# Kernel tuning notes

Measured on AMD Instinct MI355X. Metric: run time of the kernel, lower is better.

## Reference

```python
import jax, jax.numpy as jnp
import numpy as np

SCALE = 100.0
ALPHA_MEM = 0.9
ALPHA_P = 0.99
ALPHA_MEM_OUT = 0.9

@jax.custom_vjp
def spike(x):
    return (x > 0).astype(x.dtype)

def _spike_fwd(x):
    return spike(x), x

def _spike_bwd(x, g):
    return (g / (SCALE * jnp.abs(x) + 1.0) ** 2,)

spike.defvjp(_spike_fwd, _spike_bwd)

B, T, N_IN, N, N_OUT = 64, 200, 128, 2048, 20

def setup_inputs() -> dict:
    key = jax.random.key(0)
    ks = jax.random.split(key, 6)
    inputs = jax.random.normal(ks[0], (B, T, N_IN), dtype=jnp.float32)
    w = jax.random.normal(ks[1], (N, N), dtype=jnp.float32) / np.sqrt(N)
    wscale_in = 1.0 - ALPHA_MEM
    w_in = jax.random.normal(ks[2], (N_IN, N), dtype=jnp.float32) * (wscale_in / np.sqrt(N_IN))
    wscale_out = 1.0 - ALPHA_MEM_OUT
    w_out = jax.random.normal(ks[3], (N, N_OUT), dtype=jnp.float32) * (wscale_out / np.sqrt(N))
    w_signs = jnp.sign(jax.random.normal(ks[4], (N,), dtype=jnp.float32))
    p = 0.1 * jax.random.normal(ks[5], (N,), dtype=jnp.float32)
    return {"inputs": inputs, "w": w, "w_in": w_in, "w_out": w_out,
            "w_signs": w_signs, "p": p}

def reference(inputs, w, w_in, w_out, w_signs, p):
    dt = inputs.dtype
    h1 = jnp.einsum('btc,cn->btn', inputs, w_in)          # [B,T,N]
    rec_w = w_signs[:, None] * jnp.abs(w)                  # [N,N]
    depr = (p < 0).astype(dt)                              # [N]

    def step(carry, h1_t):
        mem, w_p = carry
        mthr = mem - 1.0
        out = spike(mthr)
        rst = jax.lax.stop_gradient((mthr > 0).astype(dt))
        syn_p = jnp.einsum('bn,no->bo', out * (1.0 + w_p), rec_w)
        w_p_new = w_p * ALPHA_P + out * p * (1.0 + depr * w_p)
        mem_new = ALPHA_MEM * mem + h1_t + syn_p - rst
        return (mem_new, w_p_new), out

    zeros = jnp.zeros((h1.shape[0], rec_w.shape[0]), dtype=dt)
    _, spk = jax.lax.scan(step, (zeros, zeros), jnp.swapaxes(h1, 0, 1))
    spk_rec = jnp.swapaxes(spk, 0, 1)                      # [B,T,N]

    h2 = jnp.einsum('btn,no->bto', spk_rec, w_out)         # [B,T,O]

    def out_step(o, h2_t):
        o2 = ALPHA_MEM_OUT * o + h2_t
        return o2, o2

    o0 = jnp.zeros((h2.shape[0], h2.shape[2]), dtype=dt)
    _, outs = jax.lax.scan(out_step, o0, jnp.swapaxes(h2, 0, 1))
    return jnp.swapaxes(outs, 0, 1)                        # [B,T,O]
```

## Files before the change

### kernel.cpp

```cpp
#include <hip/hip_runtime.h>

#define BB   64
#define TT   200
#define NIN  128
#define NN   2048
#define NOUT 20

#define S    8
#define NWIN 25
#define ACAP 64
#define BCAP 128

typedef __attribute__((ext_vector_type(8))) short short8;
typedef __attribute__((ext_vector_type(4))) float f32x4;

__device__ __forceinline__ void bf16split(float x, ushort& h, ushort& l) {
    unsigned u = __float_as_uint(x);
    unsigned hb = (u + 0x7FFFu + ((u >> 16) & 1u)) >> 16;
    h = (ushort)hb;
    float xh = __uint_as_float(hb << 16);
    float xl = x - xh;
    unsigned v = __float_as_uint(xl);
    l = (ushort)((v + 0x7FFFu + ((v >> 16) & 1u)) >> 16);
}

__global__ __launch_bounds__(256) void repack_a(
    const float* __restrict__ X, ushort* __restrict__ Ap)
{
    const int blk  = blockIdx.x;
    const int tid  = threadIdx.x;
    const int kc   = tid >> 6;
    const int lane = tid & 63;
    const int lr   = lane & 15, lg = lane >> 4;

    const float* src = X + (size_t)(blk * 16 + lr) * NIN + kc * 32 + lg * 8;
    float f[8];
    *(float4*)(f)     = *(const float4*)(src);
    *(float4*)(f + 4) = *(const float4*)(src + 4);

    short8 hv, lv;
    #pragma unroll
    for (int j = 0; j < 8; ++j) {
        ushort h, l;
        bf16split(f[j], h, l);
        hv[j] = (short)h; lv[j] = (short)l;
    }
    ushort* dst = Ap + (size_t)(blk * 4 + kc) * 1024 + lane * 8;
    *(short8*)(dst)       = hv;
    *(short8*)(dst + 512) = lv;
}

__global__ __launch_bounds__(256) void repack_b(
    const float* __restrict__ W, ushort* __restrict__ Bp)
{
    const int blk  = blockIdx.x;
    const int tid  = threadIdx.x;
    const int kc   = tid >> 6;
    const int lane = tid & 63;
    const int lr   = lane & 15, lg = lane >> 4;

    const float* src = W + (size_t)(kc * 32 + lg * 8) * NN + blk * 16 + lr;
    float f[8];
    #pragma unroll
    for (int j = 0; j < 8; ++j) f[j] = src[(size_t)j * NN];

    short8 hv, lv;
    #pragma unroll
    for (int j = 0; j < 8; ++j) {
        ushort h, l;
        bf16split(f[j], h, l);
        hv[j] = (short)h; lv[j] = (short)l;
    }
    ushort* dst = Bp + (size_t)(blk * 4 + kc) * 1024 + lane * 8;
    *(short8*)(dst)       = hv;
    *(short8*)(dst + 512) = lv;
}

__global__ __launch_bounds__(256, 2) void h1_mfma(
    const ushort* __restrict__ Ap, const ushort* __restrict__ Bp,
    float* __restrict__ C)
{
    const int tid  = threadIdx.x;
    const int w_   = tid >> 6, lane = tid & 63;
    const int lr   = lane & 15, lg = lane >> 4;
    const int m0   = blockIdx.y * 128, n0 = blockIdx.x * 128;
    const int wr   = (w_ >> 1) * 64, wc = (w_ & 1) * 64;

    const ushort* pA = Ap + (size_t)((m0 + wr) >> 4) * 4096 + lane * 8;
    const ushort* pB = Bp + (size_t)((n0 + wc) >> 4) * 4096 + lane * 8;

#define LDF(p) (*(const short8*)(p))
    short8 ah[2][4], al[2][4], bh[2][4], bl[2][4];
    #pragma unroll
    for (int rb = 0; rb < 4; ++rb) {
        ah[0][rb] = LDF(pA + rb * 4096);
        al[0][rb] = LDF(pA + rb * 4096 + 512);
        bh[0][rb] = LDF(pB + rb * 4096);
        bl[0][rb] = LDF(pB + rb * 4096 + 512);
    }

    f32x4 acc[4][4];
    const f32x4 z = {0.f, 0.f, 0.f, 0.f};
    #pragma unroll
    for (int rb = 0; rb < 4; ++rb)
        #pragma unroll
        for (int cb = 0; cb < 4; ++cb) acc[rb][cb] = z;

    #pragma unroll
    for (int kc = 0; kc < 4; ++kc) {
        const int cur = kc & 1, nxt = cur ^ 1;
        if (kc < 3) {
            const int ko = (kc + 1) * 1024;
            #pragma unroll
            for (int rb = 0; rb < 4; ++rb) {
                ah[nxt][rb] = LDF(pA + rb * 4096 + ko);
                al[nxt][rb] = LDF(pA + rb * 4096 + ko + 512);
                bh[nxt][rb] = LDF(pB + rb * 4096 + ko);
                bl[nxt][rb] = LDF(pB + rb * 4096 + ko + 512);
            }
        }
        #pragma unroll
        for (int rb = 0; rb < 4; ++rb)
            #pragma unroll
            for (int cb = 0; cb < 4; ++cb) {
                acc[rb][cb] = __builtin_amdgcn_mfma_f32_16x16x32_bf16(
                    bh[cur][cb], ah[cur][rb], acc[rb][cb], 0, 0, 0);
                acc[rb][cb] = __builtin_amdgcn_mfma_f32_16x16x32_bf16(
                    bl[cur][cb], ah[cur][rb], acc[rb][cb], 0, 0, 0);
                acc[rb][cb] = __builtin_amdgcn_mfma_f32_16x16x32_bf16(
                    bh[cur][cb], al[cur][rb], acc[rb][cb], 0, 0, 0);
            }
    }
#undef LDF

    #pragma unroll
    for (int rb = 0; rb < 4; ++rb) {
        float* Crow = C + (size_t)(m0 + wr + rb * 16 + lr) * NN + n0 + wc + lg * 4;
        #pragma unroll
        for (int cb = 0; cb < 4; ++cb)
            *(f32x4*)(Crow + cb * 16) = acc[rb][cb];
    }
}

__global__ __launch_bounds__(512) void snn_scan(
    const float* __restrict__ h1, const float* __restrict__ w,
    const float* __restrict__ w_signs, const float* __restrict__ pvec,
    const float* __restrict__ w_out, float* __restrict__ out)
{
    const int b   = blockIdx.x;
    const int tid = threadIdx.x;
    const int n0  = tid << 2;

    __shared__ int   s_amask[2];
    __shared__ int   s_acnt[2][S];
    __shared__ int   s_aidx[2][S][ACAP];
    __shared__ float s_aval[2][S][ACAP];
    __shared__ int   s_bcnt[2];
    __shared__ int   s_bidx[2][BCAP];
    __shared__ float s_bval[2][BCAP];

    if (tid < 2) { s_amask[tid] = 0; s_bcnt[tid] = 0; }
    if (tid < 2 * S) ((int*)s_acnt)[tid] = 0;

    float4 mem = {0.f,0.f,0.f,0.f}, wp = {0.f,0.f,0.f,0.f};
    const float4 p4 = *(const float4*)(pvec + n0);
    const float4 sg = *(const float4*)(w_signs + n0);
    float4 depr;
    depr.x = (p4.x < 0.f) ? 1.f : 0.f;  depr.y = (p4.y < 0.f) ? 1.f : 0.f;
    depr.z = (p4.z < 0.f) ? 1.f : 0.f;  depr.w = (p4.w < 0.f) ? 1.f : 0.f;

    const float P99[S] = {1.0f, 0.99f, 0.9801f, 0.970299f, 0.96059601f,
                          0.9509900499f, 0.941480149401f, 0.93206534790699f};
    const float P99_8 = 0.9227446944279201f;

    const float* hb = h1 + (size_t)b * TT * NN + n0;
    float* outb = out + (size_t)b * TT * NOUT + tid;
    float o2 = 0.f;

    float4 PA[S], PB[S];
    #pragma unroll
    for (int j = 0; j < S; ++j) PA[j] = *(const float4*)(hb + (size_t)j * NN);
    __syncthreads();

#define RAWBAR()                                              \
    do { asm volatile("s_waitcnt lgkmcnt(0)" ::: "memory");   \
         __builtin_amdgcn_s_barrier();                        \
         asm volatile("" ::: "memory"); } while (0)

    auto window = [&](float4 (&Pc)[S], float4 (&Pf)[S], int wnd) {
        const int p  = wnd & 1;
        const int t0 = wnd * S;
        const float4 memB = mem, wpB = wp;

        #pragma unroll
        for (int j = 0; j < S; ++j) {
            const float4 a = Pc[j];
            int tp = t0 + j + S; if (tp > TT - 1) tp = TT - 1;
            Pf[j] = *(const float4*)(hb + (size_t)tp * NN);

            const float mx = fmaxf(fmaxf(mem.x, mem.y), fmaxf(mem.z, mem.w));
            if (__builtin_expect(mx > 1.f, 0)) {
                const bool f0 = mem.x > 1.f, f1 = mem.y > 1.f,
                           f2 = mem.z > 1.f, f3 = mem.w > 1.f;
                atomicOr(&s_amask[p], 1 << j);
                if (f0) { int k = atomicAdd(&s_acnt[p][j], 1);
                          if (k < ACAP) { s_aidx[p][j][k] = n0;
                                          s_aval[p][j][k] = (1.f + wp.x * P99[j]) * sg.x; } }
                if (f1) { int k = atomicAdd(&s_acnt[p][j], 1);
                          if (k < ACAP) { s_aidx[p][j][k] = n0 + 1;
                                          s_aval[p][j][k] = (1.f + wp.y * P99[j]) * sg.y; } }
                if (f2) { int k = atomicAdd(&s_acnt[p][j], 1);
                          if (k < ACAP) { s_aidx[p][j][k] = n0 + 2;
                                          s_aval[p][j][k] = (1.f + wp.z * P99[j]) * sg.z; } }
                if (f3) { int k = atomicAdd(&s_acnt[p][j], 1);
                          if (k < ACAP) { s_aidx[p][j][k] = n0 + 3;
                                          s_aval[p][j][k] = (1.f + wp.w * P99[j]) * sg.w; } }
                mem.x = fmaf(0.9f, mem.x, a.x) - (f0 ? 1.f : 0.f);
                mem.y = fmaf(0.9f, mem.y, a.y) - (f1 ? 1.f : 0.f);
                mem.z = fmaf(0.9f, mem.z, a.z) - (f2 ? 1.f : 0.f);
                mem.w = fmaf(0.9f, mem.w, a.w) - (f3 ? 1.f : 0.f);
            } else {
                mem.x = fmaf(0.9f, mem.x, a.x);
                mem.y = fmaf(0.9f, mem.y, a.y);
                mem.z = fmaf(0.9f, mem.z, a.z);
                mem.w = fmaf(0.9f, mem.w, a.w);
            }
        }

        RAWBAR();
        const int mask = s_amask[p];

        if (__builtin_expect(mask == 0, 1)) {
            wp.x *= P99_8; wp.y *= P99_8; wp.z *= P99_8; wp.w *= P99_8;
            if (tid < NOUT) {
                #pragma unroll
                for (int j = 0; j < S; ++j) {
                    o2 = 0.9f * o2;
                    outb[(size_t)(t0 + j) * NOUT] = o2;
                }
            }
            return;
        }

        const int tstar = __ffs(mask) - 1;
        mem = memB; wp = wpB;
        #pragma unroll
        for (int j = 0; j < S; ++j) {
            const float4 a = Pc[j];
            if (j < tstar) {
                mem.x = fmaf(0.9f, mem.x, a.x);
                mem.y = fmaf(0.9f, mem.y, a.y);
                mem.z = fmaf(0.9f, mem.z, a.z);
                mem.w = fmaf(0.9f, mem.w, a.w);
                wp.x *= 0.99f; wp.y *= 0.99f; wp.z *= 0.99f; wp.w *= 0.99f;
                if (tid < NOUT) { o2 = 0.9f * o2;
                                  outb[(size_t)(t0 + j) * NOUT] = o2; }
            } else if (j == tstar) {
                const bool f0 = mem.x > 1.f, f1 = mem.y > 1.f,
                           f2 = mem.z > 1.f, f3 = mem.w > 1.f;
                int cnt = s_acnt[p][j]; if (cnt > ACAP) cnt = ACAP;
                float4 syn = {0.f,0.f,0.f,0.f};
                for (int m = 0; m < cnt; ++m) {
                    const int nm = s_aidx[p][j][m];
                    const float vm = s_aval[p][j][m];
                    const float4 wr = *(const float4*)(w + (size_t)nm * NN + n0);
                    syn.x = fmaf(vm, fabsf(wr.x), syn.x);
                    syn.y = fmaf(vm, fabsf(wr.y), syn.y);
                    syn.z = fmaf(vm, fabsf(wr.z), syn.z);
                    syn.w = fmaf(vm, fabsf(wr.w), syn.w);
                }
                if (tid < NOUT) {
                    float c = 0.f;
                    for (int m = 0; m < cnt; ++m)
                        c += w_out[(size_t)s_aidx[p][j][m] * NOUT + tid];
                    o2 = 0.9f * o2 + c;
                    outb[(size_t)(t0 + j) * NOUT] = o2;
                }
                mem.x = fmaf(0.9f, mem.x, a.x) + syn.x - (f0 ? 1.f : 0.f);
                mem.y = fmaf(0.9f, mem.y, a.y) + syn.y - (f1 ? 1.f : 0.f);
                mem.z = fmaf(0.9f, mem.z, a.z) + syn.z - (f2 ? 1.f : 0.f);
                mem.w = fmaf(0.9f, mem.w, a.w) + syn.w - (f3 ? 1.f : 0.f);
                wp.x = f0 ? 0.99f*wp.x + p4.x*(1.f + depr.x*wp.x) : 0.99f*wp.x;
                wp.y = f1 ? 0.99f*wp.y + p4.y*(1.f + depr.y*wp.y) : 0.99f*wp.y;
                wp.z = f2 ? 0.99f*wp.z + p4.z*(1.f + depr.z*wp.z) : 0.99f*wp.z;
                wp.w = f3 ? 0.99f*wp.w + p4.w*(1.f + depr.w*wp.w) : 0.99f*wp.w;
            } else {
                const int par = j & 1;
                const bool f0 = mem.x > 1.f, f1 = mem.y > 1.f,
                           f2 = mem.z > 1.f, f3 = mem.w > 1.f;
                if (f0 | f1 | f2 | f3) {
                    if (f0) { int k = atomicAdd(&s_bcnt[par], 1); if (k < BCAP) {
                              s_bidx[par][k] = n0;     s_bval[par][k] = (1.f + wp.x) * sg.x; } }
                    if (f1) { int k = atomicAdd(&s_bcnt[par], 1); if (k < BCAP) {
                              s_bidx[par][k] = n0 + 1; s_bval[par][k] = (1.f + wp.y) * sg.y; } }
                    if (f2) { int k = atomicAdd(&s_bcnt[par], 1); if (k < BCAP) {
                              s_bidx[par][k] = n0 + 2; s_bval[par][k] = (1.f + wp.z) * sg.z; } }
                    if (f3) { int k = atomicAdd(&s_bcnt[par], 1); if (k < BCAP) {
                              s_bidx[par][k] = n0 + 3; s_bval[par][k] = (1.f + wp.w) * sg.w; } }
                }
                RAWBAR();
                int cnt = s_bcnt[par]; if (cnt > BCAP) cnt = BCAP;
                float4 syn = {0.f,0.f,0.f,0.f};
                for (int m = 0; m < cnt; ++m) {
                    const int nm = s_bidx[par][m];
                    const float vm = s_bval[par][m];
                    const float4 wr = *(const float4*)(w + (size_t)nm * NN + n0);
                    syn.x = fmaf(vm, fabsf(wr.x), syn.x);
                    syn.y = fmaf(vm, fabsf(wr.y), syn.y);
                    syn.z = fmaf(vm, fabsf(wr.z), syn.z);
                    syn.w = fmaf(vm, fabsf(wr.w), syn.w);
                }
                if (tid < NOUT) {
                    float c = 0.f;
                    for (int m = 0; m < cnt; ++m)
                        c += w_out[(size_t)s_bidx[par][m] * NOUT + tid];
                    o2 = 0.9f * o2 + c;
                    outb[(size_t)(t0 + j) * NOUT] = o2;
                }
                mem.x = fmaf(0.9f, mem.x, a.x) + syn.x - (f0 ? 1.f : 0.f);
                mem.y = fmaf(0.9f, mem.y, a.y) + syn.y - (f1 ? 1.f : 0.f);
                mem.z = fmaf(0.9f, mem.z, a.z) + syn.z - (f2 ? 1.f : 0.f);
                mem.w = fmaf(0.9f, mem.w, a.w) + syn.w - (f3 ? 1.f : 0.f);
                wp.x = f0 ? 0.99f*wp.x + p4.x*(1.f + depr.x*wp.x) : 0.99f*wp.x;
                wp.y = f1 ? 0.99f*wp.y + p4.y*(1.f + depr.y*wp.y) : 0.99f*wp.y;
                wp.z = f2 ? 0.99f*wp.z + p4.z*(1.f + depr.z*wp.z) : 0.99f*wp.z;
                wp.w = f3 ? 0.99f*wp.w + p4.w*(1.f + depr.w*wp.w) : 0.99f*wp.w;
                RAWBAR();
                if (tid == 0) s_bcnt[par] = 0;
            }
        }
        RAWBAR();
        if (tid < S) s_acnt[p][tid] = 0;
        else if (tid == S) s_amask[p] = 0;
    };

    for (int wnd = 0; wnd < NWIN - 1; wnd += 2) {
        window(PA, PB, wnd);
        window(PB, PA, wnd + 1);
    }
    window(PA, PB, NWIN - 1);
#undef RAWBAR
}

extern "C" void kernel_launch(void* const* d_in, const int* in_sizes, int n_in,
                              void* d_out, int out_size, void* d_ws, size_t ws_size,
                              hipStream_t stream) {
    (void)in_sizes; (void)n_in; (void)out_size; (void)ws_size;
    const float* inputs  = (const float*)d_in[0];
    const float* w       = (const float*)d_in[1];
    const float* w_in    = (const float*)d_in[2];
    const float* w_out   = (const float*)d_in[3];
    const float* w_signs = (const float*)d_in[4];
    const float* p       = (const float*)d_in[5];
    float* out = (float*)d_out;

    const size_t H1B = (size_t)BB * TT * NN * 4;
    const size_t APB = (size_t)800 * 4096 * 2;

    float*  h1 = (float*)d_ws;
    ushort* Ap = (ushort*)((char*)d_ws + H1B);
    ushort* Bp = (ushort*)((char*)d_ws + H1B + APB);

    repack_a<<<800, 256, 0, stream>>>(inputs, Ap);
    repack_b<<<128, 256, 0, stream>>>(w_in, Bp);

    dim3 gg(NN / 128, (BB * TT) / 128);
    h1_mfma<<<gg, 256, 0, stream>>>(Ap, Bp, h1);

    snn_scan<<<BB, 512, 0, stream>>>(h1, w, w_signs, p, w_out, out);
}
```

Baseline: 99.60 us.

## Split each batch's SNN scan across four workgroups with global-memory sync

The recurrent scan for each batch is split across 4 workgroups of 128 threads, each owning 512 neurons, instead of one 512-thread workgroup per batch. Spike lists and counters move from shared memory to global buffers, and the workgroups synchronise per window and per spiking step through atomic counters with spin-waits. The aim is to use more compute units and shorten per-block work on the latency-bound scan. In exchange it adds inter-block spin barriers, global atomics and fences, and relies on all 256 blocks being co-resident.

```diff
diff --git a/kernel.cpp b/kernel.cpp
--- a/kernel.cpp
+++ b/kernel.cpp
@@ -8,11 +8,25 @@
 
 #define S    8
 #define NWIN 25
-#define ACAP 64
-#define BCAP 128
+#define NCHUNK 4
+#define NLOC 512
+#define STHREADS 128
+#define SACAP 32
+#define SBCAP 64
 
 typedef __attribute__((ext_vector_type(8))) short short8;
 typedef __attribute__((ext_vector_type(4))) float f32x4;
+
+#define W0 0
+#define AC 1600
+#define W2 52800
+#define BC 65600
+#define ZTOT (1600 + 51200 + 12800 + 51200)
+__device__ int   g_sync[ZTOT];
+__device__ int   g_aidx[64 * 2 * 8 * NCHUNK * SACAP];
+__device__ float g_aval[64 * 2 * 8 * NCHUNK * SACAP];
+__device__ int   g_bidx[64 * 2 * 8 * NCHUNK * SBCAP];
+__device__ float g_bval[64 * 2 * 8 * NCHUNK * SBCAP];
 
 __device__ __forceinline__ void bf16split(float x, ushort& h, ushort& l) {
     unsigned u = __float_as_uint(x);
@@ -27,6 +41,10 @@
 __global__ __launch_bounds__(256) void repack_a(
     const float* __restrict__ X, ushort* __restrict__ Ap)
 {
+    {
+        int i = blockIdx.x * 256 + threadIdx.x;
+        if (i < ZTOT) g_sync[i] = 0;
+    }
     const int blk  = blockIdx.x;
     const int tid  = threadIdx.x;
     const int kc   = tid >> 6;
@@ -142,25 +160,20 @@
     }
 }
 
-__global__ __launch_bounds__(512) void snn_scan(
+__global__ __launch_bounds__(STHREADS) void snn_scan(
     const float* __restrict__ h1, const float* __restrict__ w,
     const float* __restrict__ w_signs, const float* __restrict__ pvec,
     const float* __restrict__ w_out, float* __restrict__ out)
 {
-    const int b   = blockIdx.x;
+    const int bid = blockIdx.x;
+    const int ch  = bid >> 6;
+    const int b   = bid & 63;
     const int tid = threadIdx.x;
-    const int n0  = tid << 2;
-
-    __shared__ int   s_amask[2];
-    __shared__ int   s_acnt[2][S];
-    __shared__ int   s_aidx[2][S][ACAP];
-    __shared__ float s_aval[2][S][ACAP];
-    __shared__ int   s_bcnt[2];
-    __shared__ int   s_bidx[2][BCAP];
-    __shared__ float s_bval[2][BCAP];
-
-    if (tid < 2) { s_amask[tid] = 0; s_bcnt[tid] = 0; }
-    if (tid < 2 * S) ((int*)s_acnt)[tid] = 0;
+    const int n0  = ch * NLOC + (tid << 2);
+
+    __shared__ int s_amask;
+    __shared__ int s_gm3;
+    if (tid == 0) s_amask = 0;
 
     float4 mem = {0.f,0.f,0.f,0.f}, wp = {0.f,0.f,0.f,0.f};
     const float4 p4 = *(const float4*)(pvec + n0);
@@ -175,6 +188,7 @@
 
     const float* hb = h1 + (size_t)b * TT * NN + n0;
     float* outb = out + (size_t)b * TT * NOUT + tid;
+    const bool douto = (ch == 0) && (tid < NOUT);
     float o2 = 0.f;
 
     float4 PA[S], PB[S];
@@ -188,9 +202,11 @@
          asm volatile("" ::: "memory"); } while (0)
 
     auto window = [&](float4 (&Pc)[S], float4 (&Pf)[S], int wnd) {
-        const int p  = wnd & 1;
-        const int t0 = wnd * S;
+        const int p    = wnd & 1;
+        const int t0   = wnd * S;
+        const int widx = b * 25 + wnd;
         const float4 memB = mem, wpB = wp;
+        bool pushed = false;
 
         #pragma unroll
         for (int j = 0; j < S; ++j) {
@@ -202,19 +218,18 @@
             if (__builtin_expect(mx > 1.f, 0)) {
                 const bool f0 = mem.x > 1.f, f1 = mem.y > 1.f,
                            f2 = mem.z > 1.f, f3 = mem.w > 1.f;
-                atomicOr(&s_amask[p], 1 << j);
-                if (f0) { int k = atomicAdd(&s_acnt[p][j], 1);
-                          if (k < ACAP) { s_aidx[p][j][k] = n0;
-                                          s_aval[p][j][k] = (1.f + wp.x * P99[j]) * sg.x; } }
-                if (f1) { int k = atomicAdd(&s_acnt[p][j], 1);
-                          if (k < ACAP) { s_aidx[p][j][k] = n0 + 1;
-                                          s_aval[p][j][k] = (1.f + wp.y * P99[j]) * sg.y; } }
-                if (f2) { int k = atomicAdd(&s_acnt[p][j], 1);
-                          if (k < ACAP) { s_aidx[p][j][k] = n0 + 2;
-                                          s_aval[p][j][k] = (1.f + wp.z * P99[j]) * sg.z; } }
-                if (f3) { int k = atomicAdd(&s_acnt[p][j], 1);
-                          if (k < ACAP) { s_aidx[p][j][k] = n0 + 3;
-                                          s_aval[p][j][k] = (1.f + wp.w * P99[j]) * sg.w; } }
+                atomicOr(&s_amask, 1 << j);
+                int* cp = &g_sync[AC + (widx * 8 + j) * 4 + ch];
+                const int ab = ((((b * 2 + p) * 8 + j) * 4 + ch)) * SACAP;
+                if (f0) { int k = atomicAdd(cp, 1); if (k < SACAP) {
+                          g_aidx[ab+k] = n0;     g_aval[ab+k] = (1.f + wp.x * P99[j]) * sg.x; } }
+                if (f1) { int k = atomicAdd(cp, 1); if (k < SACAP) {
+                          g_aidx[ab+k] = n0 + 1; g_aval[ab+k] = (1.f + wp.y * P99[j]) * sg.y; } }
+                if (f2) { int k = atomicAdd(cp, 1); if (k < SACAP) {
+                          g_aidx[ab+k] = n0 + 2; g_aval[ab+k] = (1.f + wp.z * P99[j]) * sg.z; } }
+                if (f3) { int k = atomicAdd(cp, 1); if (k < SACAP) {
+                          g_aidx[ab+k] = n0 + 3; g_aval[ab+k] = (1.f + wp.w * P99[j]) * sg.w; } }
+                pushed = true;
                 mem.x = fmaf(0.9f, mem.x, a.x) - (f0 ? 1.f : 0.f);
                 mem.y = fmaf(0.9f, mem.y, a.y) - (f1 ? 1.f : 0.f);
                 mem.z = fmaf(0.9f, mem.z, a.z) - (f2 ? 1.f : 0.f);
@@ -227,12 +242,32 @@
             }
         }
 
+        if (pushed) __threadfence();
         RAWBAR();
-        const int mask = s_amask[p];
-
-        if (__builtin_expect(mask == 0, 1)) {
+
+        if (tid == 0) {
+            const int lm = s_amask;
+            s_amask = 0;
+            int lm3 = 0;
+            #pragma unroll
+            for (int j = 0; j < S; ++j) lm3 |= ((lm >> j) & 1) << (3 * j);
+            atomicAdd(&g_sync[W0 + widx], 1 + (lm3 << 8));
+            unsigned v; int it = 0;
+            for (;;) {
+                v = (unsigned)__hip_atomic_load(&g_sync[W0 + widx],
+                        __ATOMIC_ACQUIRE, __HIP_MEMORY_SCOPE_AGENT);
+                if ((v & 255u) == NCHUNK) break;
+                __builtin_amdgcn_s_sleep(2);
+                if (++it > (1 << 20)) break;
+            }
+            s_gm3 = (int)(v >> 8);
+        }
+        RAWBAR();
+        const int gm3 = s_gm3;
+
+        if (__builtin_expect(gm3 == 0, 1)) {
             wp.x *= P99_8; wp.y *= P99_8; wp.z *= P99_8; wp.w *= P99_8;
-            if (tid < NOUT) {
+            if (douto) {
                 #pragma unroll
                 for (int j = 0; j < S; ++j) {
                     o2 = 0.9f * o2;
@@ -242,7 +277,8 @@
             return;
         }
 
-        const int tstar = __ffs(mask) - 1;
+        __threadfence();
+        const int tstar = (__ffs(gm3) - 1) / 3;
         mem = memB; wp = wpB;
         #pragma unroll
         for (int j = 0; j < S; ++j) {
@@ -253,26 +289,29 @@
                 mem.z = fmaf(0.9f, mem.z, a.z);
                 mem.w = fmaf(0.9f, mem.w, a.w);
                 wp.x *= 0.99f; wp.y *= 0.99f; wp.z *= 0.99f; wp.w *= 0.99f;
-                if (tid < NOUT) { o2 = 0.9f * o2;
-                                  outb[(size_t)(t0 + j) * NOUT] = o2; }
+                if (douto) { o2 = 0.9f * o2;
+                             outb[(size_t)(t0 + j) * NOUT] = o2; }
             } else if (j == tstar) {
                 const bool f0 = mem.x > 1.f, f1 = mem.y > 1.f,
                            f2 = mem.z > 1.f, f3 = mem.w > 1.f;
-                int cnt = s_acnt[p][j]; if (cnt > ACAP) cnt = ACAP;
                 float4 syn = {0.f,0.f,0.f,0.f};
-                for (int m = 0; m < cnt; ++m) {
-                    const int nm = s_aidx[p][j][m];
-                    const float vm = s_aval[p][j][m];
-                    const float4 wr = *(const float4*)(w + (size_t)nm * NN + n0);
-                    syn.x = fmaf(vm, fabsf(wr.x), syn.x);
-                    syn.y = fmaf(vm, fabsf(wr.y), syn.y);
-                    syn.z = fmaf(vm, fabsf(wr.z), syn.z);
-                    syn.w = fmaf(vm, fabsf(wr.w), syn.w);
-                }
-                if (tid < NOUT) {
-                    float c = 0.f;
-                    for (int m = 0; m < cnt; ++m)
-                        c += w_out[(size_t)s_aidx[p][j][m] * NOUT + tid];
+                float c = 0.f;
+                for (int cc = 0; cc < NCHUNK; ++cc) {
+                    int cnt = g_sync[AC + (widx * 8 + j) * 4 + cc];
+                    if (cnt > SACAP) cnt = SACAP;
+                    const int rb2 = ((((b * 2 + p) * 8 + j) * 4 + cc)) * SACAP;
+                    for (int m = 0; m < cnt; ++m) {
+                        const int nm = g_aidx[rb2 + m];
+                        const float vm = g_aval[rb2 + m];
+                        const float4 wr = *(const float4*)(w + (size_t)nm * NN + n0);
+                        syn.x = fmaf(vm, fabsf(wr.x), syn.x);
+                        syn.y = fmaf(vm, fabsf(wr.y), syn.y);
+                        syn.z = fmaf(vm, fabsf(wr.z), syn.z);
+                        syn.w = fmaf(vm, fabsf(wr.w), syn.w);
+                        if (douto) c += w_out[(size_t)nm * NOUT + tid];
+                    }
+                }
+                if (douto) {
                     o2 = 0.9f * o2 + c;
                     outb[(size_t)(t0 + j) * NOUT] = o2;
                 }
@@ -285,35 +324,54 @@
                 wp.z = f2 ? 0.99f*wp.z + p4.z*(1.f + depr.z*wp.z) : 0.99f*wp.z;
                 wp.w = f3 ? 0.99f*wp.w + p4.w*(1.f + depr.w*wp.w) : 0.99f*wp.w;
             } else {
-                const int par = j & 1;
                 const bool f0 = mem.x > 1.f, f1 = mem.y > 1.f,
                            f2 = mem.z > 1.f, f3 = mem.w > 1.f;
-                if (f0 | f1 | f2 | f3) {
-                    if (f0) { int k = atomicAdd(&s_bcnt[par], 1); if (k < BCAP) {
-                              s_bidx[par][k] = n0;     s_bval[par][k] = (1.f + wp.x) * sg.x; } }
-                    if (f1) { int k = atomicAdd(&s_bcnt[par], 1); if (k < BCAP) {
-                              s_bidx[par][k] = n0 + 1; s_bval[par][k] = (1.f + wp.y) * sg.y; } }
-                    if (f2) { int k = atomicAdd(&s_bcnt[par], 1); if (k < BCAP) {
-                              s_bidx[par][k] = n0 + 2; s_bval[par][k] = (1.f + wp.z) * sg.z; } }
-                    if (f3) { int k = atomicAdd(&s_bcnt[par], 1); if (k < BCAP) {
-                              s_bidx[par][k] = n0 + 3; s_bval[par][k] = (1.f + wp.w) * sg.w; } }
+                const bool sp = f0 | f1 | f2 | f3;
+                if (sp) {
+                    int* cp = &g_sync[BC + (widx * 8 + j) * 4 + ch];
+                    const int bb = ((((b * 2 + p) * 8 + j) * 4 + ch)) * SBCAP;
+                    if (f0) { int k = atomicAdd(cp, 1); if (k < SBCAP) {
+                              g_bidx[bb+k] = n0;     g_bval[bb+k] = (1.f + wp.x) * sg.x; } }
+                    if (f1) { int k = atomicAdd(cp, 1); if (k < SBCAP) {
+                              g_bidx[bb+k] = n0 + 1; g_bval[bb+k] = (1.f + wp.y) * sg.y; } }
+                    if (f2) { int k = atomicAdd(cp, 1); if (k < SBCAP) {
+                              g_bidx[bb+k] = n0 + 2; g_bval[bb+k] = (1.f + wp.z) * sg.z; } }
+                    if (f3) { int k = atomicAdd(cp, 1); if (k < SBCAP) {
+                              g_bidx[bb+k] = n0 + 3; g_bval[bb+k] = (1.f + wp.w) * sg.w; } }
+                    __threadfence();
                 }
                 RAWBAR();
-                int cnt = s_bcnt[par]; if (cnt > BCAP) cnt = BCAP;
+                if (tid == 0) {
+                    atomicAdd(&g_sync[W2 + widx * 8 + j], 1);
+                    int it = 0;
+                    for (;;) {
+                        int v = __hip_atomic_load(&g_sync[W2 + widx * 8 + j],
+                                    __ATOMIC_ACQUIRE, __HIP_MEMORY_SCOPE_AGENT);
+                        if (v == NCHUNK) break;
+                        __builtin_amdgcn_s_sleep(2);
+                        if (++it > (1 << 20)) break;
+                    }
+                }
+                RAWBAR();
+                __threadfence();
                 float4 syn = {0.f,0.f,0.f,0.f};
-                for (int m = 0; m < cnt; ++m) {
-                    const int nm = s_bidx[par][m];
-                    const float vm = s_bval[par][m];
-                    const float4 wr = *(const float4*)(w + (size_t)nm * NN + n0);
-                    syn.x = fmaf(vm, fabsf(wr.x), syn.x);
-                    syn.y = fmaf(vm, fabsf(wr.y), syn.y);
-                    syn.z = fmaf(vm, fabsf(wr.z), syn.z);
-                    syn.w = fmaf(vm, fabsf(wr.w), syn.w);
-                }
-                if (tid < NOUT) {
-                    float c = 0.f;
-                    for (int m = 0; m < cnt; ++m)
-                        c += w_out[(size_t)s_bidx[par][m] * NOUT + tid];
+                float c = 0.f;
+                for (int cc = 0; cc < NCHUNK; ++cc) {
+                    int cnt = g_sync[BC + (widx * 8 + j) * 4 + cc];
+                    if (cnt > SBCAP) cnt = SBCAP;
+                    const int rb2 = ((((b * 2 + p) * 8 + j) * 4 + cc)) * SBCAP;
+                    for (int m = 0; m < cnt; ++m) {
+                        const int nm = g_bidx[rb2 + m];
+                        const float vm = g_bval[rb2 + m];
+                        const float4 wr = *(const float4*)(w + (size_t)nm * NN + n0);
+                        syn.x = fmaf(vm, fabsf(wr.x), syn.x);
+                        syn.y = fmaf(vm, fabsf(wr.y), syn.y);
+                        syn.z = fmaf(vm, fabsf(wr.z), syn.z);
+                        syn.w = fmaf(vm, fabsf(wr.w), syn.w);
+                        if (douto) c += w_out[(size_t)nm * NOUT + tid];
+                    }
+                }
+                if (douto) {
                     o2 = 0.9f * o2 + c;
                     outb[(size_t)(t0 + j) * NOUT] = o2;
                 }
@@ -325,13 +383,8 @@
                 wp.y = f1 ? 0.99f*wp.y + p4.y*(1.f + depr.y*wp.y) : 0.99f*wp.y;
                 wp.z = f2 ? 0.99f*wp.z + p4.z*(1.f + depr.z*wp.z) : 0.99f*wp.z;
                 wp.w = f3 ? 0.99f*wp.w + p4.w*(1.f + depr.w*wp.w) : 0.99f*wp.w;
-                RAWBAR();
-                if (tid == 0) s_bcnt[par] = 0;
             }
         }
-        RAWBAR();
-        if (tid < S) s_acnt[p][tid] = 0;
-        else if (tid == S) s_amask[p] = 0;
     };
 
     for (int wnd = 0; wnd < NWIN - 1; wnd += 2) {
@@ -367,5 +420,5 @@
     dim3 gg(NN / 128, (BB * TT) / 128);
     h1_mfma<<<gg, 256, 0, stream>>>(Ap, Bp, h1);
 
-    snn_scan<<<BB, 512, 0, stream>>>(h1, w, w_signs, p, w_out, out);
-}
+    snn_scan<<<BB * NCHUNK, STHREADS, 0, stream>>>(h1, w, w_signs, p, w_out, out);
+}
```

Measured after the change: 362.3 us. 3.64x slower.

## Fuse input GEMM and scan into one kernel with per-timestep-slab flag polling

Applied to the files above, without the earlier changes.

Merges the h1 GEMM and the recurrent scan into a single launch. The first 64 blocks run the per-batch scan and the remaining 800 compute GEMM tiles. h1 rows are reordered time-major so each 256-row GEMM slab covers 4 timesteps for all batches. GEMM blocks bump a global per-slab counter when done, and scan blocks spin-poll those counters before reading each window, so the scan can start while later timesteps are still being computed. This removes one launch and the serialisation between the two phases. It relies on the scan blocks being scheduled early, uses relaxed atomics with threadfence ordering, and has a bounded spin timeout that could read stale data if producers are delayed.

```diff
diff --git a/kernel.cpp b/kernel.cpp
--- a/kernel.cpp
+++ b/kernel.cpp
@@ -11,8 +11,12 @@
 #define ACAP 64
 #define BCAP 128
 
+#define HSTRIDE (64 * NN)
+
 typedef __attribute__((ext_vector_type(8))) short short8;
 typedef __attribute__((ext_vector_type(4))) float f32x4;
+
+__device__ int g_pcnt[64];
 
 __device__ __forceinline__ void bf16split(float x, ushort& h, ushort& l) {
     unsigned u = __float_as_uint(x);
@@ -27,13 +31,16 @@
 __global__ __launch_bounds__(256) void repack_a(
     const float* __restrict__ X, ushort* __restrict__ Ap)
 {
+    if (blockIdx.x == 0 && threadIdx.x < 64) g_pcnt[threadIdx.x] = 0;
     const int blk  = blockIdx.x;
     const int tid  = threadIdx.x;
     const int kc   = tid >> 6;
     const int lane = tid & 63;
     const int lr   = lane & 15, lg = lane >> 4;
 
-    const float* src = X + (size_t)(blk * 16 + lr) * NIN + kc * 32 + lg * 8;
+    const int r  = blk * 16 + lr;
+    const int bb = r & 63, tt = r >> 6;
+    const float* src = X + ((size_t)bb * TT + tt) * NIN + kc * 32 + lg * 8;
     float f[8];
     *(float4*)(f)     = *(const float4*)(src);
     *(float4*)(f + 4) = *(const float4*)(src + 4);
@@ -76,80 +83,91 @@
     *(short8*)(dst + 512) = lv;
 }
 
-__global__ __launch_bounds__(256, 2) void h1_mfma(
+__global__ __launch_bounds__(512, 2) void fused_gemm_scan(
     const ushort* __restrict__ Ap, const ushort* __restrict__ Bp,
-    float* __restrict__ C)
-{
-    const int tid  = threadIdx.x;
-    const int w_   = tid >> 6, lane = tid & 63;
-    const int lr   = lane & 15, lg = lane >> 4;
-    const int m0   = blockIdx.y * 128, n0 = blockIdx.x * 128;
-    const int wr   = (w_ >> 1) * 64, wc = (w_ & 1) * 64;
-
-    const ushort* pA = Ap + (size_t)((m0 + wr) >> 4) * 4096 + lane * 8;
-    const ushort* pB = Bp + (size_t)((n0 + wc) >> 4) * 4096 + lane * 8;
-
-#define LDF(p) (*(const short8*)(p))
-    short8 ah[2][4], al[2][4], bh[2][4], bl[2][4];
-    #pragma unroll
-    for (int rb = 0; rb < 4; ++rb) {
-        ah[0][rb] = LDF(pA + rb * 4096);
-        al[0][rb] = LDF(pA + rb * 4096 + 512);
-        bh[0][rb] = LDF(pB + rb * 4096);
-        bl[0][rb] = LDF(pB + rb * 4096 + 512);
-    }
-
-    f32x4 acc[4][4];
-    const f32x4 z = {0.f, 0.f, 0.f, 0.f};
-    #pragma unroll
-    for (int rb = 0; rb < 4; ++rb)
-        #pragma unroll
-        for (int cb = 0; cb < 4; ++cb) acc[rb][cb] = z;
-
-    #pragma unroll
-    for (int kc = 0; kc < 4; ++kc) {
-        const int cur = kc & 1, nxt = cur ^ 1;
-        if (kc < 3) {
-            const int ko = (kc + 1) * 1024;
-            #pragma unroll
-            for (int rb = 0; rb < 4; ++rb) {
-                ah[nxt][rb] = LDF(pA + rb * 4096 + ko);
-                al[nxt][rb] = LDF(pA + rb * 4096 + ko + 512);
-                bh[nxt][rb] = LDF(pB + rb * 4096 + ko);
-                bl[nxt][rb] = LDF(pB + rb * 4096 + ko + 512);
-            }
-        }
-        #pragma unroll
-        for (int rb = 0; rb < 4; ++rb)
-            #pragma unroll
-            for (int cb = 0; cb < 4; ++cb) {
-                acc[rb][cb] = __builtin_amdgcn_mfma_f32_16x16x32_bf16(
-                    bh[cur][cb], ah[cur][rb], acc[rb][cb], 0, 0, 0);
-                acc[rb][cb] = __builtin_amdgcn_mfma_f32_16x16x32_bf16(
-                    bl[cur][cb], ah[cur][rb], acc[rb][cb], 0, 0, 0);
-                acc[rb][cb] = __builtin_amdgcn_mfma_f32_16x16x32_bf16(
-                    bh[cur][cb], al[cur][rb], acc[rb][cb], 0, 0, 0);
-            }
-    }
-#undef LDF
-
-    #pragma unroll
-    for (int rb = 0; rb < 4; ++rb) {
-        float* Crow = C + (size_t)(m0 + wr + rb * 16 + lr) * NN + n0 + wc + lg * 4;
-        #pragma unroll
-        for (int cb = 0; cb < 4; ++cb)
-            *(f32x4*)(Crow + cb * 16) = acc[rb][cb];
-    }
-}
-
-__global__ __launch_bounds__(512) void snn_scan(
-    const float* __restrict__ h1, const float* __restrict__ w,
+    float* __restrict__ h1, const float* __restrict__ w,
     const float* __restrict__ w_signs, const float* __restrict__ pvec,
     const float* __restrict__ w_out, float* __restrict__ out)
 {
-    const int b   = blockIdx.x;
+    const int l   = blockIdx.x;
     const int tid = threadIdx.x;
-    const int n0  = tid << 2;
+
+    if (l >= 64) {
+        const int g     = l - 64;
+        const int mslab = g >> 4;
+        const int nb    = g & 15;
+        const int m0 = mslab * 256, n0 = nb * 128;
+        const int w_ = tid >> 6, lane = tid & 63;
+        const int lr = lane & 15, lg = lane >> 4;
+        const int wr = (w_ >> 1) * 64, wc = (w_ & 1) * 64;
+
+        const ushort* pA = Ap + (size_t)((m0 + wr) >> 4) * 4096 + lane * 8;
+        const ushort* pB = Bp + (size_t)((n0 + wc) >> 4) * 4096 + lane * 8;
+
+#define LDF(p) (*(const short8*)(p))
+        short8 ah[2][4], al[2][4], bh[2][4], bl[2][4];
+        #pragma unroll
+        for (int rb = 0; rb < 4; ++rb) {
+            ah[0][rb] = LDF(pA + rb * 4096);
+            al[0][rb] = LDF(pA + rb * 4096 + 512);
+            bh[0][rb] = LDF(pB + rb * 4096);
+            bl[0][rb] = LDF(pB + rb * 4096 + 512);
+        }
+
+        f32x4 acc[4][4];
+        const f32x4 z = {0.f, 0.f, 0.f, 0.f};
+        #pragma unroll
+        for (int rb = 0; rb < 4; ++rb)
+            #pragma unroll
+            for (int cb = 0; cb < 4; ++cb) acc[rb][cb] = z;
+
+        #pragma unroll
+        for (int kc = 0; kc < 4; ++kc) {
+            const int cur = kc & 1, nxt = cur ^ 1;
+            if (kc < 3) {
+                const int ko = (kc + 1) * 1024;
+                #pragma unroll
+                for (int rb = 0; rb < 4; ++rb) {
+                    ah[nxt][rb] = LDF(pA + rb * 4096 + ko);
+                    al[nxt][rb] = LDF(pA + rb * 4096 + ko + 512);
+                    bh[nxt][rb] = LDF(pB + rb * 4096 + ko);
+                    bl[nxt][rb] = LDF(pB + rb * 4096 + ko + 512);
+                }
+            }
+            #pragma unroll
+            for (int rb = 0; rb < 4; ++rb)
+                #pragma unroll
+                for (int cb = 0; cb < 4; ++cb) {
+                    acc[rb][cb] = __builtin_amdgcn_mfma_f32_16x16x32_bf16(
+                        bh[cur][cb], ah[cur][rb], acc[rb][cb], 0, 0, 0);
+                    acc[rb][cb] = __builtin_amdgcn_mfma_f32_16x16x32_bf16(
+                        bl[cur][cb], ah[cur][rb], acc[rb][cb], 0, 0, 0);
+                    acc[rb][cb] = __builtin_amdgcn_mfma_f32_16x16x32_bf16(
+                        bh[cur][cb], al[cur][rb], acc[rb][cb], 0, 0, 0);
+                }
+        }
+#undef LDF
+
+        #pragma unroll
+        for (int rb = 0; rb < 4; ++rb) {
+            float* Crow = h1 + (size_t)(m0 + wr + rb * 16 + lr) * NN
+                             + n0 + wc + lg * 4;
+            #pragma unroll
+            for (int cb = 0; cb < 4; ++cb)
+                *(f32x4*)(Crow + cb * 16) = acc[rb][cb];
+        }
+
+        __syncthreads();
+        if (tid == 0) {
+            __threadfence();
+            __hip_atomic_fetch_add(&g_pcnt[mslab], 1,
+                                   __ATOMIC_RELAXED, __HIP_MEMORY_SCOPE_AGENT);
+        }
+        return;
+    }
+
+    const int b  = l;
+    const int n0 = tid << 2;
 
     __shared__ int   s_amask[2];
     __shared__ int   s_acnt[2][S];
@@ -173,13 +191,31 @@
                           0.9509900499f, 0.941480149401f, 0.93206534790699f};
     const float P99_8 = 0.9227446944279201f;
 
-    const float* hb = h1 + (size_t)b * TT * NN + n0;
+    const float* hb = h1 + (size_t)b * NN + n0;
     float* outb = out + (size_t)b * TT * NOUT + tid;
     float o2 = 0.f;
 
+#define POLL2(i0, i1)                                                         \
+    do { if (tid == 0) {                                                      \
+            int it_ = 0;                                                      \
+            while (__hip_atomic_load(&g_pcnt[(i0)], __ATOMIC_RELAXED,         \
+                       __HIP_MEMORY_SCOPE_AGENT) < 16) {                      \
+                __builtin_amdgcn_s_sleep(8);                                  \
+                if (++it_ > (1 << 22)) break; }                               \
+            it_ = 0;                                                          \
+            while (__hip_atomic_load(&g_pcnt[(i1)], __ATOMIC_RELAXED,         \
+                       __HIP_MEMORY_SCOPE_AGENT) < 16) {                      \
+                __builtin_amdgcn_s_sleep(8);                                  \
+                if (++it_ > (1 << 22)) break; }                               \
+         }                                                                    \
+         __syncthreads(); } while (0)
+
+    POLL2(0, 1);
+
     float4 PA[S], PB[S];
     #pragma unroll
-    for (int j = 0; j < S; ++j) PA[j] = *(const float4*)(hb + (size_t)j * NN);
+    for (int j = 0; j < S; ++j)
+        PA[j] = *(const float4*)(hb + (size_t)j * HSTRIDE);
     __syncthreads();
 
 #define RAWBAR()                                              \
@@ -192,11 +228,13 @@
         const int t0 = wnd * S;
         const float4 memB = mem, wpB = wp;
 
+        if (wnd < NWIN - 1) POLL2(2 * wnd + 2, 2 * wnd + 3);
+
         #pragma unroll
         for (int j = 0; j < S; ++j) {
             const float4 a = Pc[j];
             int tp = t0 + j + S; if (tp > TT - 1) tp = TT - 1;
-            Pf[j] = *(const float4*)(hb + (size_t)tp * NN);
+            Pf[j] = *(const float4*)(hb + (size_t)tp * HSTRIDE);
 
             const float mx = fmaxf(fmaxf(mem.x, mem.y), fmaxf(mem.z, mem.w));
             if (__builtin_expect(mx > 1.f, 0)) {
@@ -340,6 +378,7 @@
     }
     window(PA, PB, NWIN - 1);
 #undef RAWBAR
+#undef POLL2
 }
 
 extern "C" void kernel_launch(void* const* d_in, const int* in_sizes, int n_in,
@@ -364,8 +403,6 @@
     repack_a<<<800, 256, 0, stream>>>(inputs, Ap);
     repack_b<<<128, 256, 0, stream>>>(w_in, Bp);
 
-    dim3 gg(NN / 128, (BB * TT) / 128);
-    h1_mfma<<<gg, 256, 0, stream>>>(Ap, Bp, h1);
-
-    snn_scan<<<BB, 512, 0, stream>>>(h1, w, w_signs, p, w_out, out);
+    fused_gemm_scan<<<864, 512, 0, stream>>>(Ap, Bp, h1, w, w_signs, p,
+                                             w_out, out);
 }
```

After: 136.2 us. 1.37x slower.
